# Optimization experiments

Measured on AMD Instinct MI355X. Metric: run time of the kernel, lower is better.

Reference implementation:

```python
import jax, jax.numpy as jnp
import numpy as np

HARMONICS = 5


def _harmonic_basis(x):
    k = jnp.arange(1, HARMONICS + 1, dtype=x.dtype)            # [H]
    kx = x[..., None] * k                                       # [B, D, H]
    sc = jnp.stack([jnp.sin(kx), jnp.cos(kx)], axis=-1)         # [B, D, H, 2]
    sc = sc.reshape(*x.shape, 2 * HARMONICS)                    # interleaved sin/cos
    ones = jnp.ones((*x.shape, 1), dtype=x.dtype)
    return jnp.concatenate([ones, sc], axis=-1)                 # [B, D, 2H+1]


def setup_inputs() -> dict:
    key = jax.random.key(0)
    k1, k2, k3 = jax.random.split(key, 3)
    B, D, F, H = 16384, 256, 11, 256
    x = jax.random.normal(k1, (B, D), dtype=jnp.float32)
    W = jax.random.normal(k2, (D, F, H), dtype=jnp.float32) * (1.0 / np.sqrt(F))
    b = jax.random.normal(k3, (D, H), dtype=jnp.float32) * 0.01
    return {"x": x, "W": W, "b": b}


def reference(x, W, b) -> jnp.ndarray:
    # basis expansion per feature, batched small GEMM, summed over features
    basis = _harmonic_basis(x)                                  # [B, D, F]
    out = jnp.einsum('bdf,dfh->bh', basis, W)                   # sum over features fused
    out = out + jnp.sum(b, axis=0)                              # sum of per-feature biases
    return out
```

## Files before the change

### kernel.cpp

```cpp
#include <hip/hip_runtime.h>
#include <hip/hip_bf16.h>


#define BDIM 16384
#define DDIM 256
#define HOUT 256
#define NKT  80
#define BM 128
#define BN 128

typedef __bf16 bf16x8 __attribute__((ext_vector_type(8)));
typedef float floatx4 __attribute__((ext_vector_type(4)));

__device__ __forceinline__ unsigned short f2bf(float f) {
    unsigned int u = __float_as_uint(f);
    return (unsigned short)((u + 0x7FFFu + ((u >> 16) & 1u)) >> 16);
}

__device__ __forceinline__ unsigned int pkbf(float a, float b) {
    __hip_bfloat162 r = __float22bfloat162_rn(make_float2(a, b));
    return *reinterpret_cast<unsigned int*>(&r);
}

__global__ void prep_kernel(const float* __restrict__ W, const float* __restrict__ bias,
                            unsigned short* __restrict__ Wfrag, float* __restrict__ c_part) {
    const int bid = blockIdx.x;
    const int t = threadIdx.x;
    if (bid < 4 * NKT) {
        const int kt = bid >> 2;
        const int sub = bid & 3;
        const int dtile = kt / 10;
        const int f = kt - dtile * 10 + 1;
        const int d0 = dtile * 32 + sub * 8;
        const float* wsrc = W + ((size_t)d0 * 11 + f) * 256 + t;
        union { unsigned short s[8]; int4 v; } buf;
#pragma unroll
        for (int dd = 0; dd < 8; ++dd)
            buf.s[dd] = f2bf(wsrc[(size_t)dd * 11 * 256]);
        *(int4*)(Wfrag + ((size_t)kt * 256 + t) * 32 + sub * 8) = buf.v;
    } else {
        const int p = bid - 4 * NKT;
        float acc = 0.f;
#pragma unroll
        for (int dd = 0; dd < 32; ++dd) {
            const int d = p * 32 + dd;
            acc += W[(size_t)(d * 11) * 256 + t] + bias[(size_t)d * 256 + t];
        }
        c_part[p * 256 + t] = acc;
    }
}

__global__ __launch_bounds__(512, 2)
void kan_gemm(const float* __restrict__ x, const unsigned short* __restrict__ Wfrag,
              const float* __restrict__ c_part, float* __restrict__ out) {
    __shared__ unsigned short Bs[6][2 * 8 * 512];

    const int t = threadIdx.x;
    const int m0 = blockIdx.x * BM;
    const int h0 = blockIdx.y * BN;

    const int lane = t & 63;
    const int wave = t >> 6;
    const int wr = wave >> 1;
    const int wc = wave & 1;
    const int l15 = lane & 15;
    const int koff = lane >> 4;

    floatx4 acc[2][4];
#pragma unroll
    for (int i = 0; i < 2; ++i)
#pragma unroll
        for (int j = 0; j < 4; ++j)
            acc[i][j] = (floatx4){0.f, 0.f, 0.f, 0.f};

    const float* xr0 = x + (size_t)(m0 + wr * 32 + l15) * DDIM + koff * 8;

    const unsigned short* bb = Wfrag + (size_t)(h0 + l15 * 1) * 0 + 0;

    float4 xn[4];
    xn[0] = *(const float4*)(xr0 + 0);
    xn[1] = *(const float4*)(xr0 + 4);
    xn[2] = *(const float4*)(xr0 + 16 * DDIM + 0);
    xn[3] = *(const float4*)(xr0 + 16 * DDIM + 4);

#pragma unroll
    for (int p = 0; p < 3; ++p) {
#pragma unroll
        for (int s = 0; s < 2; ++s) {
            const int c = wave * 2 + s;
            const int ktl = c >> 3;
            const int f = c & 7;
            const unsigned short* g = Wfrag + (size_t)(p * 2 + ktl) * 8192
                                    + (h0 + f * 16 + l15) * 32 + koff * 8;
            __builtin_amdgcn_global_load_lds((const void*)g,
                (void*)(&Bs[p][0] + c * 512), 16, 0, 0);
        }
    }

    float sc[16], cc[16], sp[16], cp[16], t2c[16];

#pragma unroll 1
    for (int dt = 0; dt < 8; ++dt) {
#pragma unroll
        for (int q = 0; q < 5; ++q) {

            if (q == 2) {
                const int dn = (dt < 7) ? dt + 1 : 7;
                xn[0] = *(const float4*)(xr0 + dn * 32 + 0);
                xn[1] = *(const float4*)(xr0 + dn * 32 + 4);
                xn[2] = *(const float4*)(xr0 + 16 * DDIM + dn * 32 + 0);
                xn[3] = *(const float4*)(xr0 + 16 * DDIM + dn * 32 + 4);
            }

            {
                int pt = dt * 5 + q + 3;
                if (pt > 39) pt = 39;
#pragma unroll
                for (int s = 0; s < 2; ++s) {
                    const int c = wave * 2 + s;
                    const int ktl = c >> 3;
                    const int f = c & 7;
                    const unsigned short* g = Wfrag + (size_t)(pt * 2 + ktl) * 8192
                                            + (h0 + f * 16 + l15) * 32 + koff * 8;
                    __builtin_amdgcn_global_load_lds((const void*)g,
                        (void*)(&Bs[(q + 3) % 5][0] + c * 512), 16, 0, 0);
                }
            }

            __builtin_amdgcn_sched_barrier(0);
            if (q == 2 || q == 3) {
                asm volatile("s_waitcnt vmcnt(10)" ::: "memory");
            } else {
                asm volatile("s_waitcnt vmcnt(6)" ::: "memory");
            }
            __builtin_amdgcn_s_barrier();
            __builtin_amdgcn_sched_barrier(0);

            if (q == 0) {
                const float xv[16] = {xn[0].x, xn[0].y, xn[0].z, xn[0].w,
                                      xn[1].x, xn[1].y, xn[1].z, xn[1].w,
                                      xn[2].x, xn[2].y, xn[2].z, xn[2].w,
                                      xn[3].x, xn[3].y, xn[3].z, xn[3].w};
#pragma unroll
                for (int g = 0; g < 16; ++g) {
                    __sincosf(xv[g], &sc[g], &cc[g]);
                    t2c[g] = cc[g] + cc[g];
                    sp[g] = 0.f;
                    cp[g] = 1.f;
                }
            }

#pragma unroll
            for (int s = 0; s < 2; ++s) {
                const float* src = s ? cc : sc;

                union { unsigned int u[4]; bf16x8 v; } a0, a1;
#pragma unroll
                for (int p = 0; p < 4; ++p) {
                    a0.u[p] = pkbf(src[2 * p], src[2 * p + 1]);
                    a1.u[p] = pkbf(src[8 + 2 * p], src[8 + 2 * p + 1]);
                }

                const unsigned short* fb = &Bs[q][(s * 8 + wc * 4) * 512 + lane * 8];
                const bf16x8 b0 = *(const bf16x8*)(fb);
                const bf16x8 b1 = *(const bf16x8*)(fb + 512);
                const bf16x8 b2 = *(const bf16x8*)(fb + 1024);
                const bf16x8 b3 = *(const bf16x8*)(fb + 1536);

                acc[0][0] = __builtin_amdgcn_mfma_f32_16x16x32_bf16(a0.v, b0, acc[0][0], 0, 0, 0);
                acc[1][0] = __builtin_amdgcn_mfma_f32_16x16x32_bf16(a1.v, b0, acc[1][0], 0, 0, 0);
                acc[0][1] = __builtin_amdgcn_mfma_f32_16x16x32_bf16(a0.v, b1, acc[0][1], 0, 0, 0);
                acc[1][1] = __builtin_amdgcn_mfma_f32_16x16x32_bf16(a1.v, b1, acc[1][1], 0, 0, 0);
                acc[0][2] = __builtin_amdgcn_mfma_f32_16x16x32_bf16(a0.v, b2, acc[0][2], 0, 0, 0);
                acc[1][2] = __builtin_amdgcn_mfma_f32_16x16x32_bf16(a1.v, b2, acc[1][2], 0, 0, 0);
                acc[0][3] = __builtin_amdgcn_mfma_f32_16x16x32_bf16(a0.v, b3, acc[0][3], 0, 0, 0);
                acc[1][3] = __builtin_amdgcn_mfma_f32_16x16x32_bf16(a1.v, b3, acc[1][3], 0, 0, 0);

                if (s == 1 && q < 4) {
#pragma unroll
                    for (int g = 0; g < 16; ++g) {
                        const float ns = t2c[g] * sc[g] - sp[g];
                        const float nc = t2c[g] * cc[g] - cp[g];
                        sp[g] = sc[g]; cp[g] = cc[g];
                        sc[g] = ns;   cc[g] = nc;
                    }
                }
            }
        }
    }

    asm volatile("s_waitcnt vmcnt(0)" ::: "memory");

    float cj[4];
#pragma unroll
    for (int j = 0; j < 4; ++j) {
        const int col = h0 + wc * 64 + j * 16 + l15;
        float s = 0.f;
#pragma unroll
        for (int q = 0; q < 8; ++q) s += c_part[q * 256 + col];
        cj[j] = s;
    }
#pragma unroll
    for (int i = 0; i < 2; ++i) {
        const int row0 = m0 + wr * 32 + i * 16 + koff * 4;
#pragma unroll
        for (int j = 0; j < 4; ++j) {
            const int col = h0 + wc * 64 + j * 16 + l15;
#pragma unroll
            for (int r = 0; r < 4; ++r)
                out[(size_t)(row0 + r) * HOUT + col] = acc[i][j][r] + cj[j];
        }
    }
}

extern "C" void kernel_launch(void* const* d_in, const int* in_sizes, int n_in,
                              void* d_out, int out_size, void* d_ws, size_t ws_size,
                              hipStream_t stream) {
    const float* x = (const float*)d_in[0];
    const float* W = (const float*)d_in[1];
    const float* b = (const float*)d_in[2];
    float* out = (float*)d_out;

    unsigned short* Wfrag = (unsigned short*)d_ws;
    float* c_part = (float*)((char*)d_ws + (size_t)NKT * 256 * 32 * 2);

    prep_kernel<<<4 * NKT + 8, 256, 0, stream>>>(W, b, Wfrag, c_part);
    kan_gemm<<<dim3(BDIM / BM, HOUT / BN), 512, 0, stream>>>(x, Wfrag, c_part, out);
}
```

Baseline: 102.4 us.

## Switch to fp16 MFMA with packed half2 harmonic recurrence and hardware sincos

Converts the weight fragments and basis operands from bf16 to fp16 and uses the f16 MFMA instruction. The harmonic recurrence now runs as packed half2 angle-addition math, which removes the per-step float-to-bf16 packing. Initial sin/cos come straight from v_sin_f32/v_cos_f32 on a pre-scaled argument. The intent is to cut VALU work between MFMAs, at the cost of fp16 error that grows across the recurrence and reduced accuracy of the hardware sin for large arguments.

```diff
diff --git a/kernel.cpp b/kernel.cpp
--- a/kernel.cpp
+++ b/kernel.cpp
@@ -1,5 +1,6 @@
 #include <hip/hip_runtime.h>
 #include <hip/hip_bf16.h>
+#include <hip/hip_fp16.h>
 
 
 #define BDIM 16384
@@ -9,17 +10,23 @@
 #define BM 128
 #define BN 128
 
-typedef __bf16 bf16x8 __attribute__((ext_vector_type(8)));
+typedef _Float16 halfx8 __attribute__((ext_vector_type(8)));
 typedef float floatx4 __attribute__((ext_vector_type(4)));
 
-__device__ __forceinline__ unsigned short f2bf(float f) {
-    unsigned int u = __float_as_uint(f);
-    return (unsigned short)((u + 0x7FFFu + ((u >> 16) & 1u)) >> 16);
-}
-
-__device__ __forceinline__ unsigned int pkbf(float a, float b) {
-    __hip_bfloat162 r = __float22bfloat162_rn(make_float2(a, b));
-    return *reinterpret_cast<unsigned int*>(&r);
+__device__ __forceinline__ unsigned short f2h(float f) {
+    union { _Float16 h; unsigned short u; } v;
+    v.h = (_Float16)f;
+    return v.u;
+}
+
+#define INV2PI 0.15915494309189535f
+
+__device__ __forceinline__ void hwsincos(float x, float* s, float* c) {
+    const float r = x * INV2PI;
+    float sv, cv;
+    asm("v_sin_f32 %0, %1" : "=v"(sv) : "v"(r));
+    asm("v_cos_f32 %0, %1" : "=v"(cv) : "v"(r));
+    *s = sv; *c = cv;
 }
 
 __global__ void prep_kernel(const float* __restrict__ W, const float* __restrict__ bias,
@@ -36,7 +43,7 @@
         union { unsigned short s[8]; int4 v; } buf;
 #pragma unroll
         for (int dd = 0; dd < 8; ++dd)
-            buf.s[dd] = f2bf(wsrc[(size_t)dd * 11 * 256]);
+            buf.s[dd] = f2h(wsrc[(size_t)dd * 11 * 256]);
         *(int4*)(Wfrag + ((size_t)kt * 256 + t) * 32 + sub * 8) = buf.v;
     } else {
         const int p = bid - 4 * NKT;
@@ -74,8 +81,6 @@
             acc[i][j] = (floatx4){0.f, 0.f, 0.f, 0.f};
 
     const float* xr0 = x + (size_t)(m0 + wr * 32 + l15) * DDIM + koff * 8;
-
-    const unsigned short* bb = Wfrag + (size_t)(h0 + l15 * 1) * 0 + 0;
 
     float4 xn[4];
     xn[0] = *(const float4*)(xr0 + 0);
@@ -97,7 +102,7 @@
         }
     }
 
-    float sc[16], cc[16], sp[16], cp[16], t2c[16];
+    __half2 s1h[8], c1h[8], skh[8], ckh[8];
 
 #pragma unroll 1
     for (int dt = 0; dt < 8; ++dt) {
@@ -142,47 +147,52 @@
                                       xn[2].x, xn[2].y, xn[2].z, xn[2].w,
                                       xn[3].x, xn[3].y, xn[3].z, xn[3].w};
 #pragma unroll
-                for (int g = 0; g < 16; ++g) {
-                    __sincosf(xv[g], &sc[g], &cc[g]);
-                    t2c[g] = cc[g] + cc[g];
-                    sp[g] = 0.f;
-                    cp[g] = 1.f;
+                for (int p = 0; p < 8; ++p) {
+                    float s0, c0, s1, c1;
+                    hwsincos(xv[2 * p], &s0, &c0);
+                    hwsincos(xv[2 * p + 1], &s1, &c1);
+                    const __half2 sh = __floats2half2_rn(s0, s1);
+                    const __half2 ch = __floats2half2_rn(c0, c1);
+                    s1h[p] = sh; c1h[p] = ch;
+                    skh[p] = sh; ckh[p] = ch;
                 }
             }
 
 #pragma unroll
             for (int s = 0; s < 2; ++s) {
-                const float* src = s ? cc : sc;
-
-                union { unsigned int u[4]; bf16x8 v; } a0, a1;
-#pragma unroll
-                for (int p = 0; p < 4; ++p) {
-                    a0.u[p] = pkbf(src[2 * p], src[2 * p + 1]);
-                    a1.u[p] = pkbf(src[8 + 2 * p], src[8 + 2 * p + 1]);
+                union { __half2 h2[4]; halfx8 v; } a0, a1;
+                if (s == 0) {
+#pragma unroll
+                    for (int p = 0; p < 4; ++p) { a0.h2[p] = skh[p]; a1.h2[p] = skh[p + 4]; }
+                } else {
+#pragma unroll
+                    for (int p = 0; p < 4; ++p) { a0.h2[p] = ckh[p]; a1.h2[p] = ckh[p + 4]; }
                 }
 
                 const unsigned short* fb = &Bs[q][(s * 8 + wc * 4) * 512 + lane * 8];
-                const bf16x8 b0 = *(const bf16x8*)(fb);
-                const bf16x8 b1 = *(const bf16x8*)(fb + 512);
-                const bf16x8 b2 = *(const bf16x8*)(fb + 1024);
-                const bf16x8 b3 = *(const bf16x8*)(fb + 1536);
-
-                acc[0][0] = __builtin_amdgcn_mfma_f32_16x16x32_bf16(a0.v, b0, acc[0][0], 0, 0, 0);
-                acc[1][0] = __builtin_amdgcn_mfma_f32_16x16x32_bf16(a1.v, b0, acc[1][0], 0, 0, 0);
-                acc[0][1] = __builtin_amdgcn_mfma_f32_16x16x32_bf16(a0.v, b1, acc[0][1], 0, 0, 0);
-                acc[1][1] = __builtin_amdgcn_mfma_f32_16x16x32_bf16(a1.v, b1, acc[1][1], 0, 0, 0);
-                acc[0][2] = __builtin_amdgcn_mfma_f32_16x16x32_bf16(a0.v, b2, acc[0][2], 0, 0, 0);
-                acc[1][2] = __builtin_amdgcn_mfma_f32_16x16x32_bf16(a1.v, b2, acc[1][2], 0, 0, 0);
-                acc[0][3] = __builtin_amdgcn_mfma_f32_16x16x32_bf16(a0.v, b3, acc[0][3], 0, 0, 0);
-                acc[1][3] = __builtin_amdgcn_mfma_f32_16x16x32_bf16(a1.v, b3, acc[1][3], 0, 0, 0);
+                const halfx8 b0 = *(const halfx8*)(fb);
+                const halfx8 b1 = *(const halfx8*)(fb + 512);
+                const halfx8 b2 = *(const halfx8*)(fb + 1024);
+                const halfx8 b3 = *(const halfx8*)(fb + 1536);
+
+                acc[0][0] = __builtin_amdgcn_mfma_f32_16x16x32_f16(a0.v, b0, acc[0][0], 0, 0, 0);
+                acc[1][0] = __builtin_amdgcn_mfma_f32_16x16x32_f16(a1.v, b0, acc[1][0], 0, 0, 0);
+                acc[0][1] = __builtin_amdgcn_mfma_f32_16x16x32_f16(a0.v, b1, acc[0][1], 0, 0, 0);
+                acc[1][1] = __builtin_amdgcn_mfma_f32_16x16x32_f16(a1.v, b1, acc[1][1], 0, 0, 0);
+                acc[0][2] = __builtin_amdgcn_mfma_f32_16x16x32_f16(a0.v, b2, acc[0][2], 0, 0, 0);
+                acc[1][2] = __builtin_amdgcn_mfma_f32_16x16x32_f16(a1.v, b2, acc[1][2], 0, 0, 0);
+                acc[0][3] = __builtin_amdgcn_mfma_f32_16x16x32_f16(a0.v, b3, acc[0][3], 0, 0, 0);
+                acc[1][3] = __builtin_amdgcn_mfma_f32_16x16x32_f16(a1.v, b3, acc[1][3], 0, 0, 0);
 
                 if (s == 1 && q < 4) {
 #pragma unroll
-                    for (int g = 0; g < 16; ++g) {
-                        const float ns = t2c[g] * sc[g] - sp[g];
-                        const float nc = t2c[g] * cc[g] - cp[g];
-                        sp[g] = sc[g]; cp[g] = cc[g];
-                        sc[g] = ns;   cc[g] = nc;
+                    for (int p = 0; p < 8; ++p) {
+                        const __half2 t0 = __hmul2(ckh[p], s1h[p]);
+                        const __half2 t1 = __hmul2(skh[p], s1h[p]);
+                        const __half2 ns = __hfma2(skh[p], c1h[p], t0);
+                        const __half2 nc = __hfma2(ckh[p], c1h[p], __hneg2(t1));
+                        skh[p] = ns;
+                        ckh[p] = nc;
                     }
                 }
             }
```

Result: faster. 97.24 us (-5.0%).
